# Kernel optimization log

Hardware: AMD Instinct MI355X
Metric: run time of the kernel (lower is better)

## Reference

```python
import jax, jax.numpy as jnp
import numpy as np

EMBED_DIM = 1024
NUM_HEADS = 16
HEAD_DIM = EMBED_DIM // NUM_HEADS
N_PATCHES = 220
ROPE_BASE = 10000.0
EPS = 1e-6


def rms_norm(x, g):
    # x: [..., d]
    rms = jnp.sqrt(jnp.mean(x * x, axis=-1, keepdims=True) + EPS)
    return g * (x / rms)


def apply_rope(x):
    # torchtune-style interleaved RoPE. x: [b, s, h, d]
    b, s, h, d = x.shape
    theta = 1.0 / (ROPE_BASE ** (jnp.arange(0, d, 2, dtype=jnp.float32) / d))  # [d/2]
    ang = jnp.arange(s, dtype=jnp.float32)[:, None] * theta[None, :]           # [s, d/2]
    cos = jnp.cos(ang)[None, :, None, :]
    sin = jnp.sin(ang)[None, :, None, :]
    xs = x.reshape(b, s, h, d // 2, 2)
    x0, x1 = xs[..., 0], xs[..., 1]
    out = jnp.stack([x0 * cos - x1 * sin, x1 * cos + x0 * sin], axis=-1)
    return out.reshape(b, s, h, d).astype(x.dtype)


def attention_block(x, w_qkv, w_proj, b_proj, q_gain, k_gain):
    # x: [N, S, C]; one SDPA branch (shared by spatial & temporal paths)
    N, S, C = x.shape
    H, D = NUM_HEADS, HEAD_DIM
    qkv = jnp.einsum('nsc,ec->nse', x, w_qkv).reshape(N, S, 3, H, D)
    q, k, v = qkv[:, :, 0], qkv[:, :, 1], qkv[:, :, 2]  # [N, S, H, D]
    q = apply_rope(rms_norm(q, q_gain))
    k = apply_rope(rms_norm(k, k_gain))
    scale = 1.0 / jnp.sqrt(jnp.float32(D))
    scores = jnp.einsum('nqhd,nkhd->nhqk', q, k) * scale
    attn = jax.nn.softmax(scores, axis=-1)
    out = jnp.einsum('nhqk,nkhd->nqhd', attn, v).reshape(N, S, C)
    return jnp.einsum('nsc,ec->nse', out, w_proj) + b_proj


def setup_inputs() -> dict:
    key = jax.random.key(0)
    ks = jax.random.split(key, 8)
    E = EMBED_DIM
    sd = 1.0 / np.sqrt(E)
    x = jax.random.normal(ks[0], (4, 5280, E), dtype=jnp.float32)
    w_sqkv = jax.random.uniform(ks[1], (3 * E, E), jnp.float32, -sd, sd)
    w_sproj = jax.random.uniform(ks[2], (E, E), jnp.float32, -sd, sd)
    b_sproj = jax.random.uniform(ks[3], (E,), jnp.float32, -sd, sd)
    w_tqkv = jax.random.uniform(ks[4], (3 * E, E), jnp.float32, -sd, sd)
    w_tproj = jax.random.uniform(ks[5], (E, E), jnp.float32, -sd, sd)
    b_tproj = jax.random.uniform(ks[6], (E,), jnp.float32, -sd, sd)
    g = jnp.ones((HEAD_DIM,), jnp.float32)
    return {
        'x': x,
        'w_sqkv': w_sqkv, 'w_sproj': w_sproj, 'b_sproj': b_sproj,
        'w_tqkv': w_tqkv, 'w_tproj': w_tproj, 'b_tproj': b_tproj,
        'sq_gain': g, 'sk_gain': g, 'tq_gain': g, 'tk_gain': g,
    }


def reference(x, w_sqkv, w_sproj, b_sproj, w_tqkv, w_tproj, b_tproj,
              sq_gain, sk_gain, tq_gain, tk_gain):
    B, T, C = x.shape
    P = N_PATCHES
    F = T // P
    # spatial attention per frame: (b f) p c
    xs = x.reshape(B, F, P, C).reshape(B * F, P, C)
    out_s = attention_block(xs, w_sqkv, w_sproj, b_sproj, sq_gain, sk_gain)
    # temporal attention per patch: (b p) f c
    xt = out_s.reshape(B, F, P, C).transpose(0, 2, 1, 3).reshape(B * P, F, C)
    out_t = attention_block(xt, w_tqkv, w_tproj, b_tproj, tq_gain, tk_gain)
    # (b p) f c -> b (f p) c
    out = out_t.reshape(B, P, F, C).transpose(0, 2, 1, 3).reshape(B, F * P, C)
    return out
```

## Files before the change

### kernel.cpp

```cpp
#include <hip/hip_runtime.h>

typedef _Float16 f16;
typedef _Float16 f16x8 __attribute__((ext_vector_type(8)));
typedef f16x8 f16x8a __attribute__((may_alias));
typedef float f32x4 __attribute__((ext_vector_type(4)));

#define NTOK 21120
#define SCALE_Q 0.18033688f

__device__ __forceinline__ void gll16(const void* g, void* l) {
  __builtin_amdgcn_global_load_lds(
      (const __attribute__((address_space(1))) unsigned int*)g,
      (__attribute__((address_space(3))) unsigned int*)l, 16, 0, 0);
}

__device__ __forceinline__ unsigned int pack2(float a, float b) {
  union { f16 h[2]; unsigned int u; } c;
  c.h[0] = (f16)a; c.h[1] = (f16)b;
  return c.u;
}
__device__ __forceinline__ unsigned short f2h(float a) {
  union { f16 h; unsigned short u; } c; c.h = (f16)a; return c.u;
}

__global__ __launch_bounds__(256) void cast_kernel(
    const float* __restrict__ in, unsigned short* __restrict__ out, int n4) {
  int i = blockIdx.x * 256 + threadIdx.x;
  if (i >= n4) return;
  float4 v = ((const float4*)in)[i];
  uint2 o;
  o.x = pack2(v.x, v.y);
  o.y = pack2(v.z, v.w);
  ((uint2*)out)[i] = o;
}

__global__ __launch_bounds__(256) void rope_table_kernel(float2* tabS, float2* tabT) {
  int t = blockIdx.x * 256 + threadIdx.x;
  const float lb = logf(10000.0f) * (1.0f / 32.0f);
  if (t < 220 * 32) {
    int s = t >> 5, i = t & 31;
    float theta = expf(-(float)i * lb);
    float ang = (float)s * theta;
    tabS[t] = make_float2(cosf(ang), sinf(ang));
  } else if (t < 220 * 32 + 24 * 32) {
    int u = t - 220 * 32;
    int s = u >> 5, i = u & 31;
    float theta = expf(-(float)i * lb);
    float ang = (float)s * theta;
    tabT[u] = make_float2(cosf(ang), sinf(ang));
  }
}

__global__ __launch_bounds__(256) void gemm_bt(
    const unsigned short* __restrict__ A, const unsigned short* __restrict__ B,
    const float* __restrict__ bias, void* __restrict__ C,
    int M, int N, int K, int outmode,
    const float2* __restrict__ tab, const float* __restrict__ gq,
    const float* __restrict__ gk, int mode) {
  __shared__ __align__(16) unsigned short sh[16384];
  unsigned short* As = sh;
  unsigned short* Bs = sh + 8192;
  const int tid = threadIdx.x;
  const int w = tid >> 6, lane = tid & 63;
  const int l15 = lane & 15, quad = lane >> 4;
  const int wr = w >> 1, wc = w & 1;

  const int ntn = N >> 7;
  const int stride = ntn << 3;
  const int g = blockIdx.x / stride, r = blockIdx.x % stride;
  const int tn = r % ntn, tm = g * 8 + r / ntn;

  f32x4 acc[4][4];
#pragma unroll
  for (int a = 0; a < 4; ++a)
#pragma unroll
    for (int b = 0; b < 4; ++b) acc[a][b] = (f32x4){0.f, 0.f, 0.f, 0.f};

  const int srow = tid >> 3;
  const int schk = tid & 7;
  const size_t arow0 = (size_t)tm * 128;
  const size_t brow0 = (size_t)tn * 128;
  const int nk = K >> 6;

  for (int kt = 0; kt < nk; ++kt) {
    __syncthreads();
    const int kb = kt << 6;
#pragma unroll
    for (int rd = 0; rd < 4; ++rd) {
      int row = rd * 32 + srow;
      int sc = (schk ^ (row & 7)) * 8;
      gll16(A + (arow0 + row) * K + kb + sc, (char*)As + rd * 4096 + tid * 16);
      gll16(B + (brow0 + row) * K + kb + sc, (char*)Bs + rd * 4096 + tid * 16);
    }
    __syncthreads();
#pragma unroll
    for (int kk = 0; kk < 2; ++kk) {
      f16x8 af[4], bf[4];
#pragma unroll
      for (int mt = 0; mt < 4; ++mt) {
        int ra = wr * 64 + mt * 16 + l15;
        af[mt] = *(const f16x8a*)((const char*)As + ra * 128 + (((kk * 4 + quad) ^ (ra & 7)) * 16));
        int rb = wc * 64 + mt * 16 + l15;
        bf[mt] = *(const f16x8a*)((const char*)Bs + rb * 128 + (((kk * 4 + quad) ^ (rb & 7)) * 16));
      }
#pragma unroll
      for (int mt = 0; mt < 4; ++mt)
#pragma unroll
        for (int nt = 0; nt < 4; ++nt)
          acc[mt][nt] = __builtin_amdgcn_mfma_f32_16x16x32_f16(af[mt], bf[nt], acc[mt][nt], 0, 0, 0);
    }
  }

  float bv[4];
#pragma unroll
  for (int nt = 0; nt < 4; ++nt) bv[nt] = 0.f;
  if (outmode == 1 || outmode == 2) {
#pragma unroll
    for (int nt = 0; nt < 4; ++nt) bv[nt] = bias[tn * 128 + wc * 64 + nt * 16 + l15];
  }

  if (outmode == 2) {
    float* shf = (float*)sh;
#pragma unroll
    for (int mt = 0; mt < 4; ++mt) {
      __syncthreads();
#pragma unroll
      for (int nt = 0; nt < 4; ++nt)
#pragma unroll
        for (int rg = 0; rg < 4; ++rg)
          shf[(wr * 16 + quad * 4 + rg) * 132 + wc * 64 + nt * 16 + l15] = acc[mt][nt][rg] + bv[nt];
      __syncthreads();
      int l = tid >> 3, c8 = tid & 7;
      int grow = tm * 128 + ((l >> 4) << 6) + mt * 16 + (l & 15);
      float4* dst = (float4*)((float*)C + (size_t)grow * N + tn * 128 + c8 * 16);
      const float4* srcp = (const float4*)(shf + l * 132 + c8 * 16);
#pragma unroll
      for (int c = 0; c < 4; ++c) dst[c] = srcp[c];
    }
    return;
  }

  if (outmode == 3 && tn < 16) {
    const int qtile = tn < 8;
    const float* gg = qtile ? gq : gk;
    float* shf = (float*)sh;
    const int sub = tid & 3, pr = tid >> 2;
    const int l = pr >> 1, head = pr & 1;
#pragma unroll
    for (int mt = 0; mt < 4; ++mt) {
      __syncthreads();
#pragma unroll
      for (int nt = 0; nt < 4; ++nt)
#pragma unroll
        for (int rg = 0; rg < 4; ++rg)
          shf[(wr * 16 + quad * 4 + rg) * 132 + wc * 64 + nt * 16 + l15] = acc[mt][nt][rg];
      __syncthreads();
      int grow = tm * 128 + ((l >> 4) << 6) + mt * 16 + (l & 15);
      int pos = (mode == 0) ? (grow % 220) : ((grow / 220) % 24);
      float v[16];
      const float4* vsrc = (const float4*)(shf + l * 132 + head * 64 + sub * 16);
#pragma unroll
      for (int c = 0; c < 4; ++c) {
        float4 t4 = vsrc[c];
        v[c * 4 + 0] = t4.x; v[c * 4 + 1] = t4.y; v[c * 4 + 2] = t4.z; v[c * 4 + 3] = t4.w;
      }
      float ssq = 0.f;
#pragma unroll
      for (int j = 0; j < 16; ++j) ssq += v[j] * v[j];
      ssq += __shfl_xor(ssq, 1);
      ssq += __shfl_xor(ssq, 2);
      float rr = rsqrtf(ssq * (1.0f / 64.0f) + 1e-6f);
      if (qtile) rr *= SCALE_Q;
      const float2* cs = tab + pos * 32 + sub * 8;
      const float2* g2 = (const float2*)gg + sub * 8;
      unsigned int o8[8];
#pragma unroll
      for (int jj = 0; jj < 8; ++jj) {
        float2 c = cs[jj], gp = g2[jj];
        float a = v[2 * jj] * rr * gp.x, b = v[2 * jj + 1] * rr * gp.y;
        o8[jj] = pack2(a * c.x - b * c.y, b * c.x + a * c.y);
      }
      unsigned short* dstp = (unsigned short*)C + (size_t)grow * N + tn * 128 + head * 64 + sub * 16;
      ((uint4*)dstp)[0] = ((const uint4*)o8)[0];
      ((uint4*)dstp)[1] = ((const uint4*)o8)[1];
    }
    return;
  }

  unsigned short* Cs = (unsigned short*)C;
#pragma unroll
  for (int p = 0; p < 2; ++p) {
    __syncthreads();
#pragma unroll
    for (int mi = 0; mi < 2; ++mi) {
      int mt = p * 2 + mi;
      int rl = wr * 32 + mi * 16 + quad * 4;
#pragma unroll
      for (int nt = 0; nt < 4; ++nt) {
        int cl = wc * 64 + nt * 16 + l15;
#pragma unroll
        for (int rg = 0; rg < 4; ++rg)
          sh[(rl + rg) * 136 + cl] = f2h(acc[mt][nt][rg] + bv[nt]);
      }
    }
    __syncthreads();
#pragma unroll
    for (int c = 0; c < 4; ++c) {
      int rl = c * 16 + (tid >> 4), cx = tid & 15;
      int grow = tm * 128 + ((rl >> 5) << 6) + p * 32 + (rl & 31);
      uint4 v = *(const uint4*)&sh[rl * 136 + cx * 8];
      *(uint4*)&Cs[(size_t)grow * N + tn * 128 + cx * 8] = v;
    }
  }
}

__global__ __launch_bounds__(256) void attn_spatial(
    const unsigned short* __restrict__ qkv, unsigned short* __restrict__ aout) {
  __shared__ __align__(16) unsigned short sh[30720];
  unsigned short* Kls = sh;
  unsigned short* Vt = sh + 8192;
  unsigned short* P = sh + 22528;
  const int tid = threadIdx.x;
  const int w = tid >> 6, lane = tid & 63;
  const int l15 = lane & 15, quad = lane >> 4;
  const int n = blockIdx.x >> 4, h = blockIdx.x & 15;
  const size_t tb = (size_t)n * 220;
  const unsigned short* qbase = qkv + tb * 3072 + h * 64;

  f16x8 aq[4][2];
#pragma unroll
  for (int mt = 0; mt < 4; ++mt) {
    int row = w * 64 + mt * 16 + l15;
    if (row > 219) row = 219;
#pragma unroll
    for (int c = 0; c < 2; ++c)
      aq[mt][c] = *(const f16x8a*)(qbase + (size_t)row * 3072 + c * 32 + quad * 8);
  }
  if (tid < 220) {
    const uint4* src = (const uint4*)(qbase + (size_t)tid * 3072 + 2048);
    uint4 vv[8];
#pragma unroll
    for (int c = 0; c < 8; ++c) vv[c] = src[c];
    const unsigned short* us = (const unsigned short*)vv;
#pragma unroll
    for (int d = 0; d < 64; ++d) Vt[d * 224 + tid] = us[d];
  } else if (tid < 224) {
#pragma unroll
    for (int d = 0; d < 64; ++d) Vt[d * 224 + tid] = 0;
  }

  float lsum[4][4];
  f32x4 o[4][4];
#pragma unroll
  for (int mt = 0; mt < 4; ++mt)
#pragma unroll
    for (int rg = 0; rg < 4; ++rg) lsum[mt][rg] = 0.f;
#pragma unroll
  for (int mt = 0; mt < 4; ++mt)
#pragma unroll
    for (int nt = 0; nt < 4; ++nt) o[mt][nt] = (f32x4){0.f, 0.f, 0.f, 0.f};

  const int xr = (l15 & 3) ^ ((l15 >> 2) & 3);
  unsigned short* Pw = P + w * 2048;

  for (int half = 0; half < 2; ++half) {
    const int k0 = half * 128;
    const int nslot = half ? 736 : 1024;
#pragma unroll
    for (int k = 0; k < 4; ++k) {
      int slot = k * 256 + tid;
      if (slot < nslot) {
        int rl = slot >> 3, c = slot & 7;
        gll16(qbase + (size_t)(k0 + rl) * 3072 + 1024 + ((c ^ (rl & 7)) * 8),
              (char*)Kls + k * 4096 + w * 1024);
      }
    }
    __syncthreads();
    const int nci = half ? 3 : 4;
    for (int ci = 0; ci < nci; ++ci) {
      const int cig = half * 4 + ci;
      f16x8 bk[2][2];
#pragma unroll
      for (int ct = 0; ct < 2; ++ct) {
        int rl = ci * 32 + ct * 16 + l15;
#pragma unroll
        for (int c = 0; c < 2; ++c)
          bk[ct][c] = *(const f16x8a*)((const char*)Kls + rl * 128 + (((quad + 4 * c) ^ (rl & 7)) * 16));
      }
      f32x4 sc[4][2];
#pragma unroll
      for (int mt = 0; mt < 4; ++mt)
#pragma unroll
        for (int ct = 0; ct < 2; ++ct) {
          f32x4 z = (f32x4){0.f, 0.f, 0.f, 0.f};
          z = __builtin_amdgcn_mfma_f32_16x16x32_f16(aq[mt][0], bk[ct][0], z, 0, 0, 0);
          sc[mt][ct] = __builtin_amdgcn_mfma_f32_16x16x32_f16(aq[mt][1], bk[ct][1], z, 0, 0, 0);
        }
      const int okk = (cig * 32 + 16 + l15) < 220;
#pragma unroll
      for (int mt = 0; mt < 4; ++mt)
#pragma unroll
        for (int rg = 0; rg < 4; ++rg) {
          float p0 = exp2f(sc[mt][0][rg]);
          float p1 = okk ? exp2f(sc[mt][1][rg]) : 0.0f;
          lsum[mt][rg] += p0 + p1;
          int xw = quad ^ rg;
          unsigned short* pb = Pw + (mt * 16 + quad * 4 + rg) * 32;
          pb[(((l15 >> 3) ^ xw) * 8) + (l15 & 7)] = f2h(p0);
          pb[(((2 + (l15 >> 3)) ^ xw) * 8) + (l15 & 7)] = f2h(p1);
        }
      __asm__ volatile("s_waitcnt lgkmcnt(0)" ::: "memory");
      f16x8 ap[4], bv[4];
#pragma unroll
      for (int mt = 0; mt < 4; ++mt)
        ap[mt] = *(const f16x8a*)((const char*)Pw + (mt * 16 + l15) * 64 + (quad ^ xr) * 16);
#pragma unroll
      for (int nt = 0; nt < 4; ++nt)
        bv[nt] = *(const f16x8a*)((const char*)Vt + (nt * 16 + l15) * 448 + cig * 64 + quad * 16);
#pragma unroll
      for (int mt = 0; mt < 4; ++mt)
#pragma unroll
        for (int nt = 0; nt < 4; ++nt)
          o[mt][nt] = __builtin_amdgcn_mfma_f32_16x16x32_f16(ap[mt], bv[nt], o[mt][nt], 0, 0, 0);
    }
    __syncthreads();
  }

#pragma unroll
  for (int mt = 0; mt < 4; ++mt)
#pragma unroll
    for (int rg = 0; rg < 4; ++rg) {
      float l = lsum[mt][rg];
      l += __shfl_xor(l, 1);
      l += __shfl_xor(l, 2);
      l += __shfl_xor(l, 4);
      l += __shfl_xor(l, 8);
      int s = w * 64 + mt * 16 + quad * 4 + rg;
      if (s < 220) {
        float inv = 1.0f / l;
        unsigned short* dst = aout + (tb + s) * 1024 + h * 64;
#pragma unroll
        for (int nt = 0; nt < 4; ++nt) dst[nt * 16 + l15] = f2h(o[mt][nt][rg] * inv);
      }
    }
}

__global__ __launch_bounds__(256) void attn_temporal(
    const unsigned short* __restrict__ qkv, unsigned short* __restrict__ aout) {
  __shared__ __align__(16) unsigned short sh[14336];
  const int tid = threadIdx.x;
  const int w = tid >> 6, lane = tid & 63;
  const int l15 = lane & 15, quad = lane >> 4;
  const int b = blockIdx.x / 880;
  const int rem = blockIdx.x % 880;
  const int p = rem >> 2, hq = rem & 3;
  const int h = hq * 4 + w;
  unsigned short* Vtw = sh + w * 2560;
  unsigned short* Pw = sh + 10240 + w * 1024;
  const unsigned short* base = qkv + ((size_t)(b * 24) * 220 + p) * 3072 + h * 64;
  const size_t fs = (size_t)220 * 3072;

  {
    int r = lane >> 1, hf = lane & 1;
    if (r < 24) {
      const uint4* src = (const uint4*)(base + r * fs + 2048 + hf * 32);
      uint4 vv[4];
#pragma unroll
      for (int c = 0; c < 4; ++c) vv[c] = src[c];
      const unsigned short* us = (const unsigned short*)vv;
#pragma unroll
      for (int j = 0; j < 32; ++j) Vtw[(hf * 32 + j) * 40 + r] = us[j];
    } else {
#pragma unroll
      for (int j = 0; j < 32; ++j) Vtw[(hf * 32 + j) * 40 + r] = 0;
    }
  }
  f16x8 aq[2][2], bk[2][2];
#pragma unroll
  for (int mt = 0; mt < 2; ++mt) {
    int row = mt * 16 + l15;
    if (row > 23) row = 23;
#pragma unroll
    for (int c = 0; c < 2; ++c)
      aq[mt][c] = *(const f16x8a*)(base + row * fs + c * 32 + quad * 8);
  }
#pragma unroll
  for (int ct = 0; ct < 2; ++ct) {
    int row = ct * 16 + l15;
    if (row > 23) row = 23;
#pragma unroll
    for (int c = 0; c < 2; ++c)
      bk[ct][c] = *(const f16x8a*)(base + row * fs + 1024 + c * 32 + quad * 8);
  }
  f32x4 sc[2][2];
#pragma unroll
  for (int mt = 0; mt < 2; ++mt)
#pragma unroll
    for (int ct = 0; ct < 2; ++ct) {
      f32x4 z = (f32x4){0.f, 0.f, 0.f, 0.f};
      z = __builtin_amdgcn_mfma_f32_16x16x32_f16(aq[mt][0], bk[ct][0], z, 0, 0, 0);
      sc[mt][ct] = __builtin_amdgcn_mfma_f32_16x16x32_f16(aq[mt][1], bk[ct][1], z, 0, 0, 0);
    }
  const int xr = (l15 & 3) ^ ((l15 >> 2) & 3);
  const int okk = l15 < 8;
  float lr[2][4];
#pragma unroll
  for (int mt = 0; mt < 2; ++mt)
#pragma unroll
    for (int rg = 0; rg < 4; ++rg) {
      float p0 = exp2f(sc[mt][0][rg]);
      float p1 = okk ? exp2f(sc[mt][1][rg]) : 0.0f;
      float rs = p0 + p1;
      rs += __shfl_xor(rs, 1);
      rs += __shfl_xor(rs, 2);
      rs += __shfl_xor(rs, 4);
      rs += __shfl_xor(rs, 8);
      lr[mt][rg] = rs;
      int xw = quad ^ rg;
      unsigned short* pb = Pw + (mt * 16 + quad * 4 + rg) * 32;
      pb[(((l15 >> 3) ^ xw) * 8) + (l15 & 7)] = f2h(p0);
      pb[(((2 + (l15 >> 3)) ^ xw) * 8) + (l15 & 7)] = f2h(p1);
    }
  __asm__ volatile("s_waitcnt lgkmcnt(0)" ::: "memory");
  f16x8 ap[2], bv[4];
#pragma unroll
  for (int mt = 0; mt < 2; ++mt)
    ap[mt] = *(const f16x8a*)((const char*)Pw + (mt * 16 + l15) * 64 + (quad ^ xr) * 16);
#pragma unroll
  for (int nt = 0; nt < 4; ++nt)
    bv[nt] = *(const f16x8a*)((const char*)Vtw + (nt * 16 + l15) * 80 + quad * 16);
  f32x4 o[2][4];
#pragma unroll
  for (int mt = 0; mt < 2; ++mt)
#pragma unroll
    for (int nt = 0; nt < 4; ++nt) {
      f32x4 z = (f32x4){0.f, 0.f, 0.f, 0.f};
      o[mt][nt] = __builtin_amdgcn_mfma_f32_16x16x32_f16(ap[mt], bv[nt], z, 0, 0, 0);
    }
#pragma unroll
  for (int mt = 0; mt < 2; ++mt)
#pragma unroll
    for (int rg = 0; rg < 4; ++rg) {
      int s = mt * 16 + quad * 4 + rg;
      if (s < 24) {
        float inv = 1.0f / lr[mt][rg];
        unsigned short* dst = aout + ((size_t)(b * 24 + s) * 220 + p) * 1024 + h * 64;
#pragma unroll
        for (int nt = 0; nt < 4; ++nt) dst[nt * 16 + l15] = f2h(o[mt][nt][rg] * inv);
      }
    }
}

extern "C" void kernel_launch(void* const* d_in, const int* in_sizes, int n_in,
                              void* d_out, int out_size, void* d_ws, size_t ws_size,
                              hipStream_t stream) {
  (void)in_sizes; (void)n_in; (void)out_size; (void)ws_size;
  const float* x = (const float*)d_in[0];
  const float* wsqkv = (const float*)d_in[1];
  const float* wsproj = (const float*)d_in[2];
  const float* bsproj = (const float*)d_in[3];
  const float* wtqkv = (const float*)d_in[4];
  const float* wtproj = (const float*)d_in[5];
  const float* btproj = (const float*)d_in[6];
  const float* sqg = (const float*)d_in[7];
  const float* skg = (const float*)d_in[8];
  const float* tqg = (const float*)d_in[9];
  const float* tkg = (const float*)d_in[10];

  char* ws = (char*)d_ws;
  size_t off = 0;
  auto alloc = [&](size_t bytes) {
    char* ptr = ws + off;
    off += (bytes + 255) & ~(size_t)255;
    return ptr;
  };
  unsigned short* xb = (unsigned short*)alloc((size_t)NTOK * 1024 * 2);
  unsigned short* qkvb = (unsigned short*)alloc((size_t)NTOK * 3072 * 2);
  unsigned short* aoutb = (unsigned short*)alloc((size_t)NTOK * 1024 * 2);
  unsigned short* wsqkvb = (unsigned short*)alloc((size_t)3072 * 1024 * 2);
  unsigned short* wsprojb = (unsigned short*)alloc((size_t)1024 * 1024 * 2);
  unsigned short* wtqkvb = (unsigned short*)alloc((size_t)3072 * 1024 * 2);
  unsigned short* wtprojb = (unsigned short*)alloc((size_t)1024 * 1024 * 2);
  float2* tabS = (float2*)alloc(220 * 32 * 8);
  float2* tabT = (float2*)alloc(24 * 32 * 8);

  dim3 blk(256);
  cast_kernel<<<21120, blk, 0, stream>>>(x, xb, 5406720);
  cast_kernel<<<3072, blk, 0, stream>>>(wsqkv, wsqkvb, 786432);
  cast_kernel<<<1024, blk, 0, stream>>>(wsproj, wsprojb, 262144);
  cast_kernel<<<3072, blk, 0, stream>>>(wtqkv, wtqkvb, 786432);
  cast_kernel<<<1024, blk, 0, stream>>>(wtproj, wtprojb, 262144);
  rope_table_kernel<<<31, blk, 0, stream>>>(tabS, tabT);

  gemm_bt<<<dim3(165 * 24), blk, 0, stream>>>(xb, wsqkvb, nullptr, qkvb, NTOK, 3072, 1024, 3,
                                              tabS, sqg, skg, 0);
  attn_spatial<<<dim3(1536), blk, 0, stream>>>(qkvb, aoutb);
  gemm_bt<<<dim3(165 * 8), blk, 0, stream>>>(aoutb, wsprojb, bsproj, xb, NTOK, 1024, 1024, 1,
                                             nullptr, nullptr, nullptr, 0);
  gemm_bt<<<dim3(165 * 24), blk, 0, stream>>>(xb, wtqkvb, nullptr, qkvb, NTOK, 3072, 1024, 3,
                                              tabT, tqg, tkg, 1);
  attn_temporal<<<dim3(3520), blk, 0, stream>>>(qkvb, aoutb);
  gemm_bt<<<dim3(165 * 8), blk, 0, stream>>>(aoutb, wtprojb, btproj, (float*)d_out, NTOK, 1024, 1024, 2,
                                             nullptr, nullptr, nullptr, 0);
}
```

Measured before the change: 842.9 us.

## Fold spatial output projection into temporal QKV weights algebraically

Precomputes a combined weight W_tqkv·W_sproj (via a transpose-cast and a small GEMM) and a combined bias W_tqkv·b_sproj. The temporal QKV GEMM then consumes the spatial attention output directly, which removes the full-size spatial projection GEMM and its intermediate write and read. The QKV epilogue gains bias handling before RMS norm. The weight product is rounded to fp16, which adds some numerical error, and the small weight GEMM plus bias kernel run on every call.

```diff
diff --git a/kernel.cpp b/kernel.cpp
--- a/kernel.cpp
+++ b/kernel.cpp
@@ -32,6 +32,34 @@
   o.x = pack2(v.x, v.y);
   o.y = pack2(v.z, v.w);
   ((uint2*)out)[i] = o;
+}
+
+__global__ __launch_bounds__(256) void transpose_cast_kernel(
+    const float* __restrict__ in, unsigned short* __restrict__ out) {
+  __shared__ float tile[32][33];
+  int bx = blockIdx.x & 31, by = blockIdx.x >> 5;
+  int tx = threadIdx.x & 31, ty = threadIdx.x >> 5;
+#pragma unroll
+  for (int i = 0; i < 32; i += 8)
+    tile[ty + i][tx] = in[(size_t)(by * 32 + ty + i) * 1024 + bx * 32 + tx];
+  __syncthreads();
+#pragma unroll
+  for (int i = 0; i < 32; i += 8)
+    out[(size_t)(bx * 32 + ty + i) * 1024 + by * 32 + tx] = f2h(tile[tx][ty + i]);
+}
+
+__global__ __launch_bounds__(256) void bias_combine_kernel(
+    const float* __restrict__ w, const float* __restrict__ b, float* __restrict__ bc) {
+  int e = blockIdx.x * 256 + threadIdx.x;
+  if (e >= 3072) return;
+  const float4* wr = (const float4*)(w + (size_t)e * 1024);
+  const float4* b4 = (const float4*)b;
+  float s = 0.f;
+  for (int c = 0; c < 256; ++c) {
+    float4 wv = wr[c], bv = b4[c];
+    s += wv.x * bv.x + wv.y * bv.y + wv.z * bv.z + wv.w * bv.w;
+  }
+  bc[e] = s;
 }
 
 __global__ __launch_bounds__(256) void rope_table_kernel(float2* tabS, float2* tabT) {
@@ -114,7 +142,7 @@
   float bv[4];
 #pragma unroll
   for (int nt = 0; nt < 4; ++nt) bv[nt] = 0.f;
-  if (outmode == 1 || outmode == 2) {
+  if (bias != nullptr && outmode != 3) {
 #pragma unroll
     for (int nt = 0; nt < 4; ++nt) bv[nt] = bias[tn * 128 + wc * 64 + nt * 16 + l15];
   }
@@ -146,6 +174,18 @@
     float* shf = (float*)sh;
     const int sub = tid & 3, pr = tid >> 2;
     const int l = pr >> 1, head = pr & 1;
+    float bl[16];
+    if (bias != nullptr) {
+      const float4* bsrc = (const float4*)(bias + tn * 128 + head * 64 + sub * 16);
+#pragma unroll
+      for (int c = 0; c < 4; ++c) {
+        float4 bb = bsrc[c];
+        bl[c * 4 + 0] = bb.x; bl[c * 4 + 1] = bb.y; bl[c * 4 + 2] = bb.z; bl[c * 4 + 3] = bb.w;
+      }
+    } else {
+#pragma unroll
+      for (int j = 0; j < 16; ++j) bl[j] = 0.f;
+    }
 #pragma unroll
     for (int mt = 0; mt < 4; ++mt) {
       __syncthreads();
@@ -162,7 +202,10 @@
 #pragma unroll
       for (int c = 0; c < 4; ++c) {
         float4 t4 = vsrc[c];
-        v[c * 4 + 0] = t4.x; v[c * 4 + 1] = t4.y; v[c * 4 + 2] = t4.z; v[c * 4 + 3] = t4.w;
+        v[c * 4 + 0] = t4.x + bl[c * 4 + 0];
+        v[c * 4 + 1] = t4.y + bl[c * 4 + 1];
+        v[c * 4 + 2] = t4.z + bl[c * 4 + 2];
+        v[c * 4 + 3] = t4.w + bl[c * 4 + 3];
       }
       float ssq = 0.f;
 #pragma unroll
@@ -185,6 +228,11 @@
       ((uint4*)dstp)[1] = ((const uint4*)o8)[1];
     }
     return;
+  }
+
+  if (outmode == 3 && bias != nullptr) {
+#pragma unroll
+    for (int nt = 0; nt < 4; ++nt) bv[nt] = bias[tn * 128 + wc * 64 + nt * 16 + l15];
   }
 
   unsigned short* Cs = (unsigned short*)C;
@@ -478,26 +526,30 @@
   unsigned short* qkvb = (unsigned short*)alloc((size_t)NTOK * 3072 * 2);
   unsigned short* aoutb = (unsigned short*)alloc((size_t)NTOK * 1024 * 2);
   unsigned short* wsqkvb = (unsigned short*)alloc((size_t)3072 * 1024 * 2);
-  unsigned short* wsprojb = (unsigned short*)alloc((size_t)1024 * 1024 * 2);
+  unsigned short* wsprojTb = (unsigned short*)alloc((size_t)1024 * 1024 * 2);
   unsigned short* wtqkvb = (unsigned short*)alloc((size_t)3072 * 1024 * 2);
   unsigned short* wtprojb = (unsigned short*)alloc((size_t)1024 * 1024 * 2);
+  unsigned short* wcb = (unsigned short*)alloc((size_t)3072 * 1024 * 2);
+  float* bcb = (float*)alloc(3072 * 4);
   float2* tabS = (float2*)alloc(220 * 32 * 8);
   float2* tabT = (float2*)alloc(24 * 32 * 8);
 
   dim3 blk(256);
   cast_kernel<<<21120, blk, 0, stream>>>(x, xb, 5406720);
   cast_kernel<<<3072, blk, 0, stream>>>(wsqkv, wsqkvb, 786432);
-  cast_kernel<<<1024, blk, 0, stream>>>(wsproj, wsprojb, 262144);
   cast_kernel<<<3072, blk, 0, stream>>>(wtqkv, wtqkvb, 786432);
   cast_kernel<<<1024, blk, 0, stream>>>(wtproj, wtprojb, 262144);
+  transpose_cast_kernel<<<1024, blk, 0, stream>>>(wsproj, wsprojTb);
+  bias_combine_kernel<<<12, blk, 0, stream>>>(wtqkv, bsproj, bcb);
   rope_table_kernel<<<31, blk, 0, stream>>>(tabS, tabT);
+
+  gemm_bt<<<dim3(24 * 8), blk, 0, stream>>>(wtqkvb, wsprojTb, nullptr, wcb, 3072, 1024, 1024, 0,
+                                            nullptr, nullptr, nullptr, 0);
 
   gemm_bt<<<dim3(165 * 24), blk, 0, stream>>>(xb, wsqkvb, nullptr, qkvb, NTOK, 3072, 1024, 3,
                                               tabS, sqg, skg, 0);
   attn_spatial<<<dim3(1536), blk, 0, stream>>>(qkvb, aoutb);
-  gemm_bt<<<dim3(165 * 8), blk, 0, stream>>>(aoutb, wsprojb, bsproj, xb, NTOK, 1024, 1024, 1,
-                                             nullptr, nullptr, nullptr, 0);
-  gemm_bt<<<dim3(165 * 24), blk, 0, stream>>>(xb, wtqkvb, nullptr, qkvb, NTOK, 3072, 1024, 3,
+  gemm_bt<<<dim3(165 * 24), blk, 0, stream>>>(aoutb, wcb, bcb, qkvb, NTOK, 3072, 1024, 3,
                                               tabT, tqg, tkg, 1);
   attn_temporal<<<dim3(3520), blk, 0, stream>>>(qkvb, aoutb);
   gemm_bt<<<dim3(165 * 8), blk, 0, stream>>>(aoutb, wtprojb, btproj, (float*)d_out, NTOK, 1024, 1024, 2,
```

After: 791.7 us. 1.06x faster.
